# Kernel optimization log

Hardware: AMD Instinct MI355X
Metric: run time of the kernel (lower is better)

Reference implementation:

```python
import jax, jax.numpy as jnp
import numpy as np

D_MODEL = 1024
HEADS = 16
HEAD_DIM = D_MODEL // HEADS


def setup_inputs() -> dict:
    key = jax.random.key(0)
    k_x, k_q, k_k, k_v, k_o = jax.random.split(key, 5)
    B, S = 4, 2048
    return {
        "x": jax.random.normal(k_x, (B, S, D_MODEL), dtype=jnp.float32),
        "W_q": jax.random.normal(k_q, (D_MODEL, D_MODEL), dtype=jnp.float32),
        "W_k": jax.random.normal(k_k, (D_MODEL, D_MODEL), dtype=jnp.float32),
        "W_v": jax.random.normal(k_v, (D_MODEL, D_MODEL), dtype=jnp.float32),
        "fc_out": jax.random.normal(k_o, (D_MODEL, D_MODEL), dtype=jnp.float32),
    }


def reference(x, W_q, W_k, W_v, fc_out):
    B, S, D = x.shape
    H, Hd = HEADS, HEAD_DIM
    # QKV projections (no bias)
    Q = jnp.matmul(x, W_q)  # [B,S,D]
    K = jnp.matmul(x, W_k)
    V = jnp.matmul(x, W_v)
    # split heads -> [B,H,S,Hd]
    Qh = Q.reshape(B, S, H, Hd).transpose(0, 2, 1, 3)
    Kh = K.reshape(B, S, H, Hd).transpose(0, 2, 1, 3)
    Vh = V.reshape(B, S, H, Hd).transpose(0, 2, 1, 3)
    # full unfused attention: materialize [B,H,S,S] scores, softmax over last dim
    scores = jnp.einsum("bhqd,bhkd->bhqk", Qh, Kh) / jnp.sqrt(jnp.float32(Hd))
    attn = jax.nn.softmax(scores, axis=-1)
    head_out = jnp.einsum("bhqk,bhkd->bhqd", attn, Vh)  # [B,H,S,Hd]
    merged = head_out.transpose(0, 2, 1, 3).reshape(B, S, D)
    return jnp.matmul(merged, fc_out)
```

## Files before the change

kernel.cpp:

```cpp
#include <hip/hip_runtime.h>
#include <stdint.h>

#define MROWS 8192
#define DM    1024
#define NH    16
#define HD    64
#define SEQ   2048

typedef __bf16 bf16x8 __attribute__((ext_vector_type(8)));
typedef __bf16 bf16x4 __attribute__((ext_vector_type(4)));
typedef float  floatx4 __attribute__((ext_vector_type(4)));

#define QSCALE 0.18033688011112042f

__device__ __forceinline__ void async16(const void* g, void* l) {
  __builtin_amdgcn_global_load_lds(
      (__attribute__((address_space(1))) void*)g,
      (__attribute__((address_space(3))) void*)l,
      16, 0, 0);
}

__device__ __forceinline__ floatx4 mfma16(bf16x8 a, bf16x8 b, floatx4 c) {
  return __builtin_amdgcn_mfma_f32_16x16x32_bf16(a, b, c, 0, 0, 0);
}

template <int CTRL>
__device__ __forceinline__ float dpp_mov(float x) {
  return __builtin_bit_cast(float,
      __builtin_amdgcn_update_dpp(0, __builtin_bit_cast(int, x), CTRL, 0xF, 0xF, true));
}
__device__ __forceinline__ float red16_max(float x) {
  x = fmaxf(x, dpp_mov<0xB1>(x));
  x = fmaxf(x, dpp_mov<0x4E>(x));
  x = fmaxf(x, dpp_mov<0x124>(x));
  x = fmaxf(x, dpp_mov<0x128>(x));
  return x;
}


__global__ void __launch_bounds__(256) split_x_kernel(const float* __restrict__ x,
                                                      __bf16* __restrict__ xh,
                                                      __bf16* __restrict__ xl) {
  const int i = blockIdx.x * 256 + threadIdx.x;
  const float4 v = reinterpret_cast<const float4*>(x)[i];
  const float vv[4] = {v.x, v.y, v.z, v.w};
  bf16x4 H, L;
#pragma unroll
  for (int j = 0; j < 4; ++j) {
    const __bf16 h = (__bf16)vv[j];
    H[j] = h;
    L[j] = (__bf16)(vv[j] - (float)h);
  }
  reinterpret_cast<bf16x4*>(xh)[i] = H;
  reinterpret_cast<bf16x4*>(xl)[i] = L;
}

__global__ void __launch_bounds__(256) wtrans_kernel(const float* __restrict__ W,
                                                     __bf16* __restrict__ Th,
                                                     __bf16* __restrict__ Tl) {
  __shared__ float t[32][33];
  const int tx = threadIdx.x & 31, ty = threadIdx.x >> 5;
  const int bx = blockIdx.x & 31, by = blockIdx.x >> 5;
#pragma unroll
  for (int j = 0; j < 4; ++j) {
    const int k = by * 32 + ty + j * 8;
    t[ty + j * 8][tx] = W[(size_t)k * DM + bx * 32 + tx];
  }
  __syncthreads();
#pragma unroll
  for (int j = 0; j < 4; ++j) {
    const int n = bx * 32 + ty + j * 8;
    const int k = by * 32 + tx;
    const float v = t[tx][ty + j * 8];
    const __bf16 h = (__bf16)v;
    Th[(size_t)n * DM + k] = h;
    if (Tl) Tl[(size_t)n * DM + k] = (__bf16)(v - (float)h);
  }
}

template <int OUTMODE>
__global__ void __launch_bounds__(256) gemm_nt(const __bf16* __restrict__ Ah,
                                               const __bf16* __restrict__ Bh,
                                               void* __restrict__ C0) {
  __shared__ __align__(16) __bf16 sAh[128 * 32];
  __shared__ __align__(16) __bf16 sBh[128 * 32];

  const int tid = threadIdx.x;
  const int bm = blockIdx.x >> 3;
  const int bn = blockIdx.x & 7;
  const int m0 = bm << 7, n0 = bn << 7;
  const int w = tid >> 6;
  const int lane = tid & 63;
  const int wm = (w >> 1) << 6;
  const int wn = (w & 1) << 6;
  const int lm = lane & 15;
  const int q4 = lane >> 4;

  floatx4 acc[4][4];
  const floatx4 fz = {0.f, 0.f, 0.f, 0.f};
#pragma unroll
  for (int i = 0; i < 4; ++i)
#pragma unroll
    for (int j = 0; j < 4; ++j) acc[i][j] = fz;

  const int c0 = tid, c1 = tid + 256;
  const int row0 = c0 >> 2, cc0 = (c0 & 3) ^ ((row0 >> 1) & 3);
  const int row1 = c1 >> 2, cc1 = (c1 & 3) ^ ((row1 >> 1) & 3);

  int offA[4], offB[4];
#pragma unroll
  for (int i = 0; i < 4; ++i) {
    const int ra = wm + i * 16 + lm;
    offA[i] = ra * 32 + ((q4 ^ ((ra >> 1) & 3)) << 3);
    const int rb = wn + i * 16 + lm;
    offB[i] = rb * 32 + ((q4 ^ ((rb >> 1) & 3)) << 3);
  }

  size_t ga0 = (size_t)(m0 + row0) * DM + cc0 * 8;
  size_t gb0 = (size_t)(n0 + row0) * DM + cc0 * 8;
  size_t ga1 = (size_t)(m0 + row1) * DM + cc1 * 8;
  size_t gb1 = (size_t)(n0 + row1) * DM + cc1 * 8;

  for (int it = 0; it < 32; ++it) {
    async16(Ah + ga0, &sAh[c0 * 8]);
    async16(Bh + gb0, &sBh[c0 * 8]);
    async16(Ah + ga1, &sAh[c1 * 8]);
    async16(Bh + gb1, &sBh[c1 * 8]);
    ga0 += 32; gb0 += 32; ga1 += 32; gb1 += 32;
    __syncthreads();

    bf16x8 ah[4], bh[4];
#pragma unroll
    for (int i = 0; i < 4; ++i) {
      ah[i] = *(const bf16x8*)&sAh[offA[i]];
      bh[i] = *(const bf16x8*)&sBh[offB[i]];
    }
#pragma unroll
    for (int i = 0; i < 4; ++i)
#pragma unroll
      for (int j = 0; j < 4; ++j)
        acc[i][j] = mfma16(ah[i], bh[j], acc[i][j]);
    __syncthreads();
  }

#pragma unroll
  for (int i = 0; i < 4; ++i) {
#pragma unroll
    for (int j = 0; j < 4; ++j) {
#pragma unroll
      for (int r = 0; r < 4; ++r) {
        const int gr = m0 + wm + i * 16 + q4 * 4 + r;
        const int gc = n0 + wn + j * 16 + lm;
        const float v = acc[i][j][r];
        if constexpr (OUTMODE == 1) {
          ((float*)C0)[(size_t)gr * DM + gc] = v;
        } else {
          const int bb = gr >> 11, ss = gr & 2047;
          const int hh = gc >> 6, dd = gc & 63;
          ((__bf16*)C0)[(((size_t)(bb * NH + hh) << 6) + dd) * SEQ + ss] = (__bf16)v;
        }
      }
    }
  }
}

__global__ void __launch_bounds__(256, 2) gemm_qk(const __bf16* __restrict__ Ah,
                                                  const __bf16* __restrict__ Al,
                                                  const __bf16* __restrict__ Bqh,
                                                  const __bf16* __restrict__ Bql,
                                                  const __bf16* __restrict__ Bkh,
                                                  const __bf16* __restrict__ Bkl,
                                                  __bf16* __restrict__ Qh,
                                                  __bf16* __restrict__ Ql,
                                                  __bf16* __restrict__ Kh,
                                                  __bf16* __restrict__ Kl) {
  __shared__ __align__(16) __bf16 sAh[128 * 32];
  __shared__ __align__(16) __bf16 sAl[128 * 32];
  __shared__ __align__(16) __bf16 sQh_[128 * 32];
  __shared__ __align__(16) __bf16 sQl_[128 * 32];
  __shared__ __align__(16) __bf16 sKh_[128 * 32];
  __shared__ __align__(16) __bf16 sKl_[128 * 32];

  const int tid = threadIdx.x;
  const int bm = blockIdx.x >> 3;
  const int bn = blockIdx.x & 7;
  const int m0 = bm << 7, n0 = bn << 7;
  const int w = tid >> 6;
  const int lane = tid & 63;
  const int wm = (w >> 1) << 6;
  const int wn = (w & 1) << 6;
  const int lm = lane & 15;
  const int q4 = lane >> 4;

  floatx4 accq[4][4], acck[4][4];
  const floatx4 fz = {0.f, 0.f, 0.f, 0.f};
#pragma unroll
  for (int i = 0; i < 4; ++i)
#pragma unroll
    for (int j = 0; j < 4; ++j) { accq[i][j] = fz; acck[i][j] = fz; }

  const int c0 = tid, c1 = tid + 256;
  const int row0 = c0 >> 2, cc0 = (c0 & 3) ^ ((row0 >> 1) & 3);
  const int row1 = c1 >> 2, cc1 = (c1 & 3) ^ ((row1 >> 1) & 3);

  int offA[4], offB[4];
#pragma unroll
  for (int i = 0; i < 4; ++i) {
    const int ra = wm + i * 16 + lm;
    offA[i] = ra * 32 + ((q4 ^ ((ra >> 1) & 3)) << 3);
    const int rb = wn + i * 16 + lm;
    offB[i] = rb * 32 + ((q4 ^ ((rb >> 1) & 3)) << 3);
  }

  size_t ga0 = (size_t)(m0 + row0) * DM + cc0 * 8;
  size_t gb0 = (size_t)(n0 + row0) * DM + cc0 * 8;
  size_t ga1 = (size_t)(m0 + row1) * DM + cc1 * 8;
  size_t gb1 = (size_t)(n0 + row1) * DM + cc1 * 8;

  for (int it = 0; it < 32; ++it) {
    async16(Ah + ga0, &sAh[c0 * 8]);
    async16(Al + ga0, &sAl[c0 * 8]);
    async16(Ah + ga1, &sAh[c1 * 8]);
    async16(Al + ga1, &sAl[c1 * 8]);
    async16(Bqh + gb0, &sQh_[c0 * 8]);
    async16(Bql + gb0, &sQl_[c0 * 8]);
    async16(Bqh + gb1, &sQh_[c1 * 8]);
    async16(Bql + gb1, &sQl_[c1 * 8]);
    async16(Bkh + gb0, &sKh_[c0 * 8]);
    async16(Bkl + gb0, &sKl_[c0 * 8]);
    async16(Bkh + gb1, &sKh_[c1 * 8]);
    async16(Bkl + gb1, &sKl_[c1 * 8]);
    ga0 += 32; gb0 += 32; ga1 += 32; gb1 += 32;
    __syncthreads();

    bf16x8 ah[4], al[4];
#pragma unroll
    for (int i = 0; i < 4; ++i) {
      ah[i] = *(const bf16x8*)&sAh[offA[i]];
      al[i] = *(const bf16x8*)&sAl[offA[i]];
    }
    {
      bf16x8 bh[4], bl[4];
#pragma unroll
      for (int j = 0; j < 4; ++j) {
        bh[j] = *(const bf16x8*)&sQh_[offB[j]];
        bl[j] = *(const bf16x8*)&sQl_[offB[j]];
      }
#pragma unroll
      for (int i = 0; i < 4; ++i)
#pragma unroll
        for (int j = 0; j < 4; ++j) {
          accq[i][j] = mfma16(ah[i], bh[j], accq[i][j]);
          accq[i][j] = mfma16(ah[i], bl[j], accq[i][j]);
          accq[i][j] = mfma16(al[i], bh[j], accq[i][j]);
        }
    }
    {
      bf16x8 bh[4], bl[4];
#pragma unroll
      for (int j = 0; j < 4; ++j) {
        bh[j] = *(const bf16x8*)&sKh_[offB[j]];
        bl[j] = *(const bf16x8*)&sKl_[offB[j]];
      }
#pragma unroll
      for (int i = 0; i < 4; ++i)
#pragma unroll
        for (int j = 0; j < 4; ++j) {
          acck[i][j] = mfma16(ah[i], bh[j], acck[i][j]);
          acck[i][j] = mfma16(ah[i], bl[j], acck[i][j]);
          acck[i][j] = mfma16(al[i], bh[j], acck[i][j]);
        }
    }
    __syncthreads();
  }

#pragma unroll
  for (int i = 0; i < 4; ++i) {
#pragma unroll
    for (int j = 0; j < 4; ++j) {
#pragma unroll
      for (int r = 0; r < 4; ++r) {
        const int gr = m0 + wm + i * 16 + q4 * 4 + r;
        const int gc = n0 + wn + j * 16 + lm;
        const size_t idx = (size_t)gr * DM + gc;
        const float vq = accq[i][j][r] * QSCALE;
        const __bf16 qhv = (__bf16)vq;
        Qh[idx] = qhv;
        Ql[idx] = (__bf16)(vq - (float)qhv);
        const float vk = acck[i][j][r];
        const __bf16 khv = (__bf16)vk;
        Kh[idx] = khv;
        Kl[idx] = (__bf16)(vk - (float)khv);
      }
    }
  }
}

__global__ void __launch_bounds__(256, 3) flash_kernel(const __bf16* __restrict__ Qh,
                                                       const __bf16* __restrict__ Ql,
                                                       const __bf16* __restrict__ Kh,
                                                       const __bf16* __restrict__ Kl,
                                                       const __bf16* __restrict__ Vt,
                                                       __bf16* __restrict__ Mg) {
  __shared__ __align__(16) __bf16 sKh[64 * 64];
  __shared__ __align__(16) __bf16 sKl[64 * 64];
  __shared__ __align__(16) __bf16 sV[64 * 64];
  __shared__ __align__(16) __bf16 sP[4][32 * 72];

  const int tid = threadIdx.x;
  const int qt = blockIdx.x & 15;
  const int bh = blockIdx.x >> 4;
  const int b = bh >> 4;
  const int h = bh & 15;
  const int mq0 = b * SEQ + qt * 128;
  const int ch = h * 64;
  const int w = tid >> 6;
  const int lane = tid & 63;
  const int lm = lane & 15;
  const int q4 = lane >> 4;

  const int c0 = tid, c1 = tid + 256;
  const int r0 = c0 >> 3, e0 = ((c0 & 7) ^ (r0 & 7)) << 3;
  const int r1 = c1 >> 3, e1 = ((c1 & 7) ^ (r1 & 7)) << 3;

  bf16x8 qh[2][2], ql[2][2];
#pragma unroll
  for (int p = 0; p < 2; ++p) {
    const size_t gq0 = (size_t)(mq0 + p * 64 + r0) * DM + ch + e0;
    const size_t gq1 = (size_t)(mq0 + p * 64 + r1) * DM + ch + e1;
    async16(Qh + gq0, &sKh[c0 * 8]);
    async16(Ql + gq0, &sKl[c0 * 8]);
    async16(Qh + gq1, &sKh[c1 * 8]);
    async16(Ql + gq1, &sKl[c1 * 8]);
    __syncthreads();
    if ((w >> 1) == p) {
#pragma unroll
      for (int mi = 0; mi < 2; ++mi) {
        const int rq = (w & 1) * 32 + mi * 16 + lm;
#pragma unroll
        for (int ks = 0; ks < 2; ++ks) {
          const int oq = rq * 64 + (((ks * 4 + q4) ^ (rq & 7)) << 3);
          qh[mi][ks] = *(const bf16x8*)&sKh[oq];
          ql[mi][ks] = *(const bf16x8*)&sKl[oq];
        }
      }
    }
    __syncthreads();
  }

  int ofr[2][4];
#pragma unroll
  for (int ks = 0; ks < 2; ++ks)
#pragma unroll
    for (int t = 0; t < 4; ++t) {
      const int rk = t * 16 + lm;
      ofr[ks][t] = rk * 64 + (((ks * 4 + q4) ^ (rk & 7)) << 3);
    }

  bf16x8 ones;
#pragma unroll
  for (int j = 0; j < 8; ++j) ones[j] = (__bf16)1.0f;

  floatx4 o[2][4], lsum[2];
  const floatx4 fz = {0.f, 0.f, 0.f, 0.f};
#pragma unroll
  for (int mi = 0; mi < 2; ++mi) {
#pragma unroll
    for (int dt = 0; dt < 4; ++dt) o[mi][dt] = fz;
    lsum[mi] = fz;
  }
  float mrow[2][4];
#pragma unroll
  for (int mi = 0; mi < 2; ++mi)
#pragma unroll
    for (int r = 0; r < 4; ++r) mrow[mi][r] = -1e30f;

  size_t gk0 = (size_t)(b * SEQ + r0) * DM + ch + e0;
  size_t gk1 = (size_t)(b * SEQ + r1) * DM + ch + e1;
  size_t gv0 = (size_t)(bh * 64 + r0) * SEQ + e0;
  size_t gv1 = (size_t)(bh * 64 + r1) * SEQ + e1;

  for (int it = 0; it < 32; ++it) {
    async16(Kh + gk0, &sKh[c0 * 8]);
    async16(Kl + gk0, &sKl[c0 * 8]);
    async16(Kh + gk1, &sKh[c1 * 8]);
    async16(Kl + gk1, &sKl[c1 * 8]);
    async16(Vt + gv0, &sV[c0 * 8]);
    async16(Vt + gv1, &sV[c1 * 8]);
    gk0 += (size_t)64 * DM;
    gk1 += (size_t)64 * DM;
    gv0 += 64;
    gv1 += 64;
    __syncthreads();

    floatx4 s[2][4];
#pragma unroll
    for (int mi = 0; mi < 2; ++mi)
#pragma unroll
      for (int nt = 0; nt < 4; ++nt) s[mi][nt] = fz;
#pragma unroll
    for (int ks = 0; ks < 2; ++ks) {
#pragma unroll
      for (int nt = 0; nt < 4; ++nt) {
        const bf16x8 kh = *(const bf16x8*)&sKh[ofr[ks][nt]];
        const bf16x8 kl = *(const bf16x8*)&sKl[ofr[ks][nt]];
#pragma unroll
        for (int mi = 0; mi < 2; ++mi) {
          s[mi][nt] = mfma16(qh[mi][ks], kh, s[mi][nt]);
          s[mi][nt] = mfma16(qh[mi][ks], kl, s[mi][nt]);
          s[mi][nt] = mfma16(ql[mi][ks], kh, s[mi][nt]);
        }
      }
    }

    float mnew[2][4];
    bool upd = false;
#pragma unroll
    for (int mi = 0; mi < 2; ++mi)
#pragma unroll
      for (int r = 0; r < 4; ++r) {
        float mx = fmaxf(fmaxf(s[mi][0][r], s[mi][1][r]), fmaxf(s[mi][2][r], s[mi][3][r]));
        mx = red16_max(mx);
        mnew[mi][r] = fmaxf(mrow[mi][r], mx);
        upd = upd || (mnew[mi][r] > mrow[mi][r]);
      }
    if (__ballot(upd)) {
#pragma unroll
      for (int mi = 0; mi < 2; ++mi)
#pragma unroll
        for (int r = 0; r < 4; ++r) {
          const float a = __builtin_amdgcn_exp2f(mrow[mi][r] - mnew[mi][r]);
          mrow[mi][r] = mnew[mi][r];
          lsum[mi][r] *= a;
#pragma unroll
          for (int dt = 0; dt < 4; ++dt) o[mi][dt][r] *= a;
        }
    }
#pragma unroll
    for (int mi = 0; mi < 2; ++mi)
#pragma unroll
      for (int r = 0; r < 4; ++r) {
        const int prow = mi * 16 + q4 * 4 + r;
#pragma unroll
        for (int nt = 0; nt < 4; ++nt)
          sP[w][prow * 72 + nt * 16 + lm] =
              (__bf16)__builtin_amdgcn_exp2f(s[mi][nt][r] - mrow[mi][r]);
      }

#pragma unroll
    for (int ks = 0; ks < 2; ++ks) {
      bf16x8 a[2];
#pragma unroll
      for (int mi = 0; mi < 2; ++mi) {
        a[mi] = *(const bf16x8*)&sP[w][(mi * 16 + lm) * 72 + ks * 32 + q4 * 8];
        lsum[mi] = mfma16(a[mi], ones, lsum[mi]);
      }
#pragma unroll
      for (int dt = 0; dt < 4; ++dt) {
        const bf16x8 bv = *(const bf16x8*)&sV[ofr[ks][dt]];
#pragma unroll
        for (int mi = 0; mi < 2; ++mi)
          o[mi][dt] = mfma16(a[mi], bv, o[mi][dt]);
      }
    }
    __syncthreads();
  }

#pragma unroll
  for (int mi = 0; mi < 2; ++mi)
#pragma unroll
    for (int r = 0; r < 4; ++r) {
      const float inv = __builtin_amdgcn_rcpf(lsum[mi][r]);
      const int gr = mq0 + w * 32 + mi * 16 + q4 * 4 + r;
#pragma unroll
      for (int dt = 0; dt < 4; ++dt)
        Mg[(size_t)gr * DM + ch + dt * 16 + lm] = (__bf16)(o[mi][dt][r] * inv);
    }
}


extern "C" void kernel_launch(void* const* d_in, const int* in_sizes, int n_in,
                              void* d_out, int out_size, void* d_ws, size_t ws_size,
                              hipStream_t stream) {
  (void)in_sizes; (void)n_in; (void)out_size; (void)ws_size;
  const float* x  = (const float*)d_in[0];
  const float* Wq = (const float*)d_in[1];
  const float* Wk = (const float*)d_in[2];
  const float* Wv = (const float*)d_in[3];
  const float* fc = (const float*)d_in[4];
  float* out = (float*)d_out;

  char* base = (char*)d_ws;
  const size_t XB = (size_t)MROWS * DM * 2;
  const size_t WB = (size_t)DM * DM * 2;
  __bf16* xh  = (__bf16*)(base);
  __bf16* xl  = (__bf16*)(base + XB);
  __bf16* wqh = (__bf16*)(base + 2 * XB);
  __bf16* wql = (__bf16*)(base + 2 * XB + WB);
  __bf16* wkh = (__bf16*)(base + 2 * XB + 2 * WB);
  __bf16* wkl = (__bf16*)(base + 2 * XB + 3 * WB);
  __bf16* wvh = (__bf16*)(base + 2 * XB + 4 * WB);
  __bf16* fch = (__bf16*)(base + 2 * XB + 5 * WB);
  __bf16* Qh  = (__bf16*)(base + 2 * XB + 6 * WB);
  __bf16* Ql  = (__bf16*)(base + 3 * XB + 6 * WB);
  __bf16* Kh  = (__bf16*)(base + 4 * XB + 6 * WB);
  __bf16* Kl  = (__bf16*)(base + 5 * XB + 6 * WB);
  __bf16* Vt  = xl;
  __bf16* Mg  = xh;

  split_x_kernel<<<dim3(8192), dim3(256), 0, stream>>>(x, xh, xl);
  wtrans_kernel<<<dim3(1024), dim3(256), 0, stream>>>(Wq, wqh, wql);
  wtrans_kernel<<<dim3(1024), dim3(256), 0, stream>>>(Wk, wkh, wkl);
  wtrans_kernel<<<dim3(1024), dim3(256), 0, stream>>>(Wv, wvh, (__bf16*)nullptr);
  wtrans_kernel<<<dim3(1024), dim3(256), 0, stream>>>(fc, fch, (__bf16*)nullptr);

  gemm_qk<<<dim3(512), dim3(256), 0, stream>>>(xh, xl, wqh, wql, wkh, wkl, Qh, Ql, Kh, Kl);
  gemm_nt<3><<<dim3(512), dim3(256), 0, stream>>>(xh, wvh, (void*)Vt);

  flash_kernel<<<dim3(1024), dim3(256), 0, stream>>>(Qh, Ql, Kh, Kl, Vt, Mg);

  gemm_nt<1><<<dim3(512), dim3(256), 0, stream>>>(Mg, fch, (void*)out);
}
```

Before: 435.0 us.

## Transpose attention MFMA operands so each lane owns one query row

Swaps the A/B operands in the QK^T and PV MFMAs so the score and output tiles are transposed, putting one query row per lane instead of spreading it across 16 lanes. Row max and row sum then reduce over registers plus two cross-lane shuffles, replacing the 16-lane DPP max reduction and the extra MFMA that summed P against a ones vector. It also skips rescaling the running state unless a tile max exceeds the running max by more than 8 (log2 domain), and writes P and the output as packed bf16x4 stores. The lazy rescale allows exponentials up to 2^8 before renormalising, which lowers float headroom in exchange for fewer rescale passes.

```diff
diff --git a/kernel.cpp b/kernel.cpp
--- a/kernel.cpp
+++ b/kernel.cpp
@@ -22,19 +22,6 @@
 
 __device__ __forceinline__ floatx4 mfma16(bf16x8 a, bf16x8 b, floatx4 c) {
   return __builtin_amdgcn_mfma_f32_16x16x32_bf16(a, b, c, 0, 0, 0);
-}
-
-template <int CTRL>
-__device__ __forceinline__ float dpp_mov(float x) {
-  return __builtin_bit_cast(float,
-      __builtin_amdgcn_update_dpp(0, __builtin_bit_cast(int, x), CTRL, 0xF, 0xF, true));
-}
-__device__ __forceinline__ float red16_max(float x) {
-  x = fmaxf(x, dpp_mov<0xB1>(x));
-  x = fmaxf(x, dpp_mov<0x4E>(x));
-  x = fmaxf(x, dpp_mov<0x124>(x));
-  x = fmaxf(x, dpp_mov<0x128>(x));
-  return x;
 }
 
 
@@ -357,23 +344,14 @@
       ofr[ks][t] = rk * 64 + (((ks * 4 + q4) ^ (rk & 7)) << 3);
     }
 
-  bf16x8 ones;
-#pragma unroll
-  for (int j = 0; j < 8; ++j) ones[j] = (__bf16)1.0f;
-
-  floatx4 o[2][4], lsum[2];
+  floatx4 o[2][4];
   const floatx4 fz = {0.f, 0.f, 0.f, 0.f};
 #pragma unroll
-  for (int mi = 0; mi < 2; ++mi) {
+  for (int mi = 0; mi < 2; ++mi)
 #pragma unroll
     for (int dt = 0; dt < 4; ++dt) o[mi][dt] = fz;
-    lsum[mi] = fz;
-  }
-  float mrow[2][4];
-#pragma unroll
-  for (int mi = 0; mi < 2; ++mi)
-#pragma unroll
-    for (int r = 0; r < 4; ++r) mrow[mi][r] = -1e30f;
+  float lsum[2] = {0.f, 0.f};
+  float m[2] = {-1e30f, -1e30f};
 
   size_t gk0 = (size_t)(b * SEQ + r0) * DM + ch + e0;
   size_t gk1 = (size_t)(b * SEQ + r1) * DM + ch + e1;
@@ -393,11 +371,11 @@
     gv1 += 64;
     __syncthreads();
 
-    floatx4 s[2][4];
-#pragma unroll
-    for (int mi = 0; mi < 2; ++mi)
-#pragma unroll
-      for (int nt = 0; nt < 4; ++nt) s[mi][nt] = fz;
+    floatx4 s2[4][2];
+#pragma unroll
+    for (int nt = 0; nt < 4; ++nt)
+#pragma unroll
+      for (int mi = 0; mi < 2; ++mi) s2[nt][mi] = fz;
 #pragma unroll
     for (int ks = 0; ks < 2; ++ks) {
 #pragma unroll
@@ -406,76 +384,84 @@
         const bf16x8 kl = *(const bf16x8*)&sKl[ofr[ks][nt]];
 #pragma unroll
         for (int mi = 0; mi < 2; ++mi) {
-          s[mi][nt] = mfma16(qh[mi][ks], kh, s[mi][nt]);
-          s[mi][nt] = mfma16(qh[mi][ks], kl, s[mi][nt]);
-          s[mi][nt] = mfma16(ql[mi][ks], kh, s[mi][nt]);
+          s2[nt][mi] = mfma16(kh, qh[mi][ks], s2[nt][mi]);
+          s2[nt][mi] = mfma16(kl, qh[mi][ks], s2[nt][mi]);
+          s2[nt][mi] = mfma16(kh, ql[mi][ks], s2[nt][mi]);
         }
       }
     }
 
-    float mnew[2][4];
-    bool upd = false;
-#pragma unroll
-    for (int mi = 0; mi < 2; ++mi)
-#pragma unroll
-      for (int r = 0; r < 4; ++r) {
-        float mx = fmaxf(fmaxf(s[mi][0][r], s[mi][1][r]), fmaxf(s[mi][2][r], s[mi][3][r]));
-        mx = red16_max(mx);
-        mnew[mi][r] = fmaxf(mrow[mi][r], mx);
-        upd = upd || (mnew[mi][r] > mrow[mi][r]);
-      }
-    if (__ballot(upd)) {
-#pragma unroll
-      for (int mi = 0; mi < 2; ++mi)
+    float tm[2];
+#pragma unroll
+    for (int mi = 0; mi < 2; ++mi) {
+      float mx = fmaxf(fmaxf(s2[0][mi][0], s2[0][mi][1]),
+                       fmaxf(s2[0][mi][2], s2[0][mi][3]));
+#pragma unroll
+      for (int nt = 1; nt < 4; ++nt) {
+        mx = fmaxf(mx, fmaxf(fmaxf(s2[nt][mi][0], s2[nt][mi][1]),
+                             fmaxf(s2[nt][mi][2], s2[nt][mi][3])));
+      }
+      mx = fmaxf(mx, __shfl_xor(mx, 16));
+      mx = fmaxf(mx, __shfl_xor(mx, 32));
+      tm[mi] = mx;
+    }
+    if (__ballot((tm[0] > m[0] + 8.f) || (tm[1] > m[1] + 8.f))) {
+#pragma unroll
+      for (int mi = 0; mi < 2; ++mi) {
+        const float mn = fmaxf(m[mi], tm[mi]);
+        const float a = __builtin_amdgcn_exp2f(m[mi] - mn);
+        m[mi] = mn;
+        lsum[mi] *= a;
+#pragma unroll
+        for (int dt = 0; dt < 4; ++dt) o[mi][dt] *= a;
+      }
+    }
+
+#pragma unroll
+    for (int mi = 0; mi < 2; ++mi) {
+      float ps = 0.f;
+#pragma unroll
+      for (int nt = 0; nt < 4; ++nt) {
+        bf16x4 pk;
 #pragma unroll
         for (int r = 0; r < 4; ++r) {
-          const float a = __builtin_amdgcn_exp2f(mrow[mi][r] - mnew[mi][r]);
-          mrow[mi][r] = mnew[mi][r];
-          lsum[mi][r] *= a;
-#pragma unroll
-          for (int dt = 0; dt < 4; ++dt) o[mi][dt][r] *= a;
+          const float p = __builtin_amdgcn_exp2f(s2[nt][mi][r] - m[mi]);
+          ps += p;
+          pk[r] = (__bf16)p;
         }
-    }
-#pragma unroll
-    for (int mi = 0; mi < 2; ++mi)
-#pragma unroll
-      for (int r = 0; r < 4; ++r) {
-        const int prow = mi * 16 + q4 * 4 + r;
-#pragma unroll
-        for (int nt = 0; nt < 4; ++nt)
-          sP[w][prow * 72 + nt * 16 + lm] =
-              (__bf16)__builtin_amdgcn_exp2f(s[mi][nt][r] - mrow[mi][r]);
-      }
+        *(bf16x4*)&sP[w][(mi * 16 + lm) * 72 + nt * 16 + q4 * 4] = pk;
+      }
+      ps += __shfl_xor(ps, 16);
+      ps += __shfl_xor(ps, 32);
+      lsum[mi] += ps;
+    }
 
 #pragma unroll
     for (int ks = 0; ks < 2; ++ks) {
-      bf16x8 a[2];
-#pragma unroll
-      for (int mi = 0; mi < 2; ++mi) {
-        a[mi] = *(const bf16x8*)&sP[w][(mi * 16 + lm) * 72 + ks * 32 + q4 * 8];
-        lsum[mi] = mfma16(a[mi], ones, lsum[mi]);
-      }
+      const bf16x8 a0 = *(const bf16x8*)&sP[w][lm * 72 + ks * 32 + q4 * 8];
+      const bf16x8 a1 = *(const bf16x8*)&sP[w][(16 + lm) * 72 + ks * 32 + q4 * 8];
 #pragma unroll
       for (int dt = 0; dt < 4; ++dt) {
         const bf16x8 bv = *(const bf16x8*)&sV[ofr[ks][dt]];
-#pragma unroll
-        for (int mi = 0; mi < 2; ++mi)
-          o[mi][dt] = mfma16(a[mi], bv, o[mi][dt]);
-      }
-    }
-    __syncthreads();
-  }
-
-#pragma unroll
-  for (int mi = 0; mi < 2; ++mi)
-#pragma unroll
-    for (int r = 0; r < 4; ++r) {
-      const float inv = __builtin_amdgcn_rcpf(lsum[mi][r]);
-      const int gr = mq0 + w * 32 + mi * 16 + q4 * 4 + r;
-#pragma unroll
-      for (int dt = 0; dt < 4; ++dt)
-        Mg[(size_t)gr * DM + ch + dt * 16 + lm] = (__bf16)(o[mi][dt][r] * inv);
-    }
+        o[0][dt] = mfma16(bv, a0, o[0][dt]);
+        o[1][dt] = mfma16(bv, a1, o[1][dt]);
+      }
+    }
+    __syncthreads();
+  }
+
+#pragma unroll
+  for (int mi = 0; mi < 2; ++mi) {
+    const float inv = __builtin_amdgcn_rcpf(lsum[mi]);
+    const int gr = mq0 + w * 32 + mi * 16 + lm;
+#pragma unroll
+    for (int dt = 0; dt < 4; ++dt) {
+      bf16x4 ov;
+#pragma unroll
+      for (int r = 0; r < 4; ++r) ov[r] = (__bf16)(o[mi][dt][r] * inv);
+      *(bf16x4*)&Mg[(size_t)gr * DM + ch + dt * 16 + q4 * 4] = ov;
+    }
+  }
 }
 
 
```

New measurement: 408.0 us. 1.07x faster.
